# Kernel tuning notes

Hardware: AMD Instinct MI355X
Metric: run time of the kernel (lower is better)

The kernel has to match this reference:

```python
import jax, jax.numpy as jnp
import numpy as np

N, FIN, FOUT, K = 4096, 512, 128, 4
LRELU_ALPHA = 0.2


def setup_inputs() -> dict:
    key = jax.random.key(0)
    k1, k2, k3, k4 = jax.random.split(key, 4)
    x = jax.random.normal(k1, (N, FIN), dtype=jnp.float32)
    # binary adjacency with guaranteed self-loops so every row has a neighbor
    adj = jax.random.randint(k2, (N, N), 0, 2, dtype=jnp.int32)
    adj = jnp.maximum(adj, jnp.eye(N, dtype=jnp.int32))
    # xavier-uniform-ish init for W:(K,FIN,FOUT) and a:(K,2*FOUT,1)
    limW = float(np.sqrt(6.0 / (FIN + FOUT)))
    W = jax.random.uniform(k3, (K, FIN, FOUT), dtype=jnp.float32, minval=-limW, maxval=limW)
    lima = float(np.sqrt(6.0 / (2 * FOUT + 1)))
    a = jax.random.uniform(k4, (K, 2 * FOUT, 1), dtype=jnp.float32, minval=-lima, maxval=lima)
    return {"x": x, "adj": adj, "W": W, "a": a}


def reference(x, adj, W, a):
    # x: [N, Fin], adj: [N, N] int, W: [K, Fin, F'], a: [K, 2F', 1]
    Fout = W.shape[-1]
    h = jnp.einsum('nf,kfo->nko', x, W)          # [N, K, F'] per-head projection
    a_src = a[:, :Fout, 0]                        # [K, F'] acts on h_i
    a_dst = a[:, Fout:, 0]                        # [K, F'] acts on h_j
    # a^T [h_i || h_j] == a_src . h_i + a_dst . h_j  (no O(N^2) concat)
    e_i = jnp.einsum('nko,ko->nk', h, a_src)      # [N, K]
    e_j = jnp.einsum('nko,ko->nk', h, a_dst)      # [N, K]
    scores = e_i[:, :, None] + e_j.T[None, :, :]  # [N, K, N]
    scores = jax.nn.leaky_relu(scores, LRELU_ALPHA)
    mask = (adj != 0)[:, None, :]                 # [N, 1, N]
    scores = jnp.where(mask, scores, -jnp.inf)
    coeffs = jax.nn.softmax(scores, axis=-1)      # [N, K, N]
    # dropout is identity in eval mode
    out = jnp.einsum('nkm,mko->nko', coeffs, h)   # [N, K, F'] aggregation
    return out.reshape(out.shape[0], -1)          # concat heads -> [N, K*F']
```

## Files before the change

kernel.cpp:

```cpp
#include <hip/hip_runtime.h>
#include <hip/hip_bf16.h>

typedef float f4 __attribute__((ext_vector_type(4)));
typedef int   i4 __attribute__((ext_vector_type(4)));
typedef unsigned short us8 __attribute__((ext_vector_type(8)));
typedef short bfrag __attribute__((ext_vector_type(8)));
typedef float f16v __attribute__((ext_vector_type(16)));

constexpr int NN   = 4096;
constexpr int FINc = 512;
constexpr int FOUTc= 128;
constexpr int KHc  = 4;
constexpr int KFc  = 512;
constexpr float ALPHA = 0.2f;
constexpr float LOG2E = 1.44269504088896340736f;

static __device__ __forceinline__ unsigned short f2bf(float f) {
    unsigned u = __float_as_uint(f);
    return (unsigned short)((u + 0x7fffu + ((u >> 16) & 1u)) >> 16);
}
static __device__ __forceinline__ float bf2f(unsigned short u) {
    return __uint_as_float(((unsigned)u) << 16);
}
static __device__ __forceinline__ bfrag us2bf(us8 v) {
    union { us8 u; bfrag s; } cv; cv.u = v; return cv.s;
}


__global__ __launch_bounds__(256) void prep_kernel(const float* __restrict__ x,
                                                   const float* __restrict__ W,
                                                   unsigned short* __restrict__ xb,
                                                   unsigned short* __restrict__ WbT) {
    __shared__ float tile[32 * 132];
    const int b = blockIdx.x, t = threadIdx.x;
    if (b < 1024) {
        size_t base = ((size_t)b * 256 + t) * 8;
        f4 v0 = *(const f4*)&x[base];
        f4 v1 = *(const f4*)&x[base + 4];
        us8 o;
#pragma unroll
        for (int j = 0; j < 4; ++j) { o[j] = f2bf(v0[j]); o[4 + j] = f2bf(v1[j]); }
        *(us8*)&xb[base] = o;
    } else {
        const int wb = b - 1024;
        const int k = wb >> 4, f0 = (wb & 15) * 32;
#pragma unroll
        for (int p = 0; p < 4; ++p) {
            int fl = p * 8 + (t >> 5);
            int oc = (t & 31) * 4;
            *(f4*)&tile[fl * 132 + oc] =
                *(const f4*)&W[(size_t)k * 65536 + (size_t)(f0 + fl) * 128 + oc];
        }
        __syncthreads();
        const int o = t >> 1, fh = (t & 1) * 16;
        alignas(16) unsigned short buf[16];
#pragma unroll
        for (int j = 0; j < 16; ++j) buf[j] = f2bf(tile[(fh + j) * 132 + o]);
        unsigned short* dst = &WbT[((size_t)k * 128 + o) * FINc + f0 + fh];
        *(us8*)dst       = *(const us8*)&buf[0];
        *(us8*)(dst + 8) = *(const us8*)&buf[8];
    }
}

__global__ __launch_bounds__(256) void gemmh_bits_kernel(const unsigned short* __restrict__ xb,
                                                         const unsigned short* __restrict__ WbT,
                                                         const int* __restrict__ adj,
                                                         unsigned short* __restrict__ hB,
                                                         unsigned* __restrict__ bits) {
    __shared__ char Ax[64 * 128];
    __shared__ char Bx[64 * 128];
    const int b = blockIdx.x, t = threadIdx.x;
    if (b >= 512) {
        size_t i0 = (size_t)(b - 512) * 16384 + (size_t)t * 64;
        const int* ap = adj + i0;
        unsigned long long bb = 0ull;
#pragma unroll
        for (int c = 0; c < 16; ++c) {
            i4 v = *(const i4*)(ap + c * 4);
            unsigned n = (v[0] != 0 ? 1u : 0u) | (v[1] != 0 ? 2u : 0u)
                       | (v[2] != 0 ? 4u : 0u) | (v[3] != 0 ? 8u : 0u);
            bb |= (unsigned long long)n << (c * 4);
        }
        *(unsigned long long*)&bits[i0 >> 5] = bb;
        return;
    }
    const int wid = t >> 6, lane = t & 63;
    const int c0 = (b & 7) * 64, n0 = (b >> 3) * 64;
    const int head = c0 >> 7, ob = c0 & 127;
    const int srow = t >> 2, sseg = t & 3;
    const unsigned short* asrc = &xb[(size_t)(n0 + srow) * FINc + sseg * 16];
    const unsigned short* bsrc = &WbT[((size_t)(head * 128 + ob + srow)) * FINc + sseg * 16];
    const int rowbase = (wid & 1) * 32, colbase = (wid >> 1) * 32;
    f16v acc = {};
    for (int fc = 0; fc < FINc; fc += 64) {
        us8 a0 = *(const us8*)(asrc + fc), a1 = *(const us8*)(asrc + fc + 8);
        us8 b0 = *(const us8*)(bsrc + fc), b1 = *(const us8*)(bsrc + fc + 8);
        __syncthreads();
        {
            int byt = (sseg * 32) ^ ((srow & 7) << 4);
            char* pa = Ax + srow * 128;
            *(us8*)(pa + byt) = a0;  *(us8*)(pa + (byt ^ 16)) = a1;
            char* pb = Bx + srow * 128;
            *(us8*)(pb + byt) = b0;  *(us8*)(pb + (byt ^ 16)) = b1;
        }
        __syncthreads();
#pragma unroll
        for (int ks = 0; ks < 4; ++ks) {
            int kb = ks * 32 + ((lane >> 5) << 4);
            int ar = rowbase + (lane & 31);
            bfrag af = *(const bfrag*)(Ax + ar * 128 + (kb ^ ((ar & 7) << 4)));
            int bc = colbase + (lane & 31);
            bfrag bf = *(const bfrag*)(Bx + bc * 128 + (kb ^ ((bc & 7) << 4)));
            acc = __builtin_amdgcn_mfma_f32_32x32x16_bf16(af, bf, acc, 0, 0, 0);
        }
    }
    __syncthreads();
#pragma unroll
    for (int reg = 0; reg < 16; ++reg) {
        int row = rowbase + (reg & 3) + 8 * (reg >> 2) + 4 * (lane >> 5);
        int col = colbase + (lane & 31);
        *(unsigned short*)(Ax + row * 128 + ((col * 2) ^ ((row & 7) << 4))) = f2bf(acc[reg]);
    }
    __syncthreads();
    {
        const int col_l = t & 63;
        unsigned short* dstbase = hB + (size_t)head * 524288 + (size_t)(n0 >> 6) * 8192
                                     + (size_t)(ob + col_l) * 8;
#pragma unroll
        for (int g = 0; g < 2; ++g) {
            int o8 = (t >> 6) + g * 4;
            int ks = o8 >> 1, lg = o8 & 1;
            alignas(16) unsigned short buf[8];
#pragma unroll
            for (int j = 0; j < 8; ++j) {
                int r = o8 * 8 + j;
                buf[j] = *(const unsigned short*)(Ax + r * 128 + ((col_l * 2) ^ ((r & 7) << 4)));
            }
            *(us8*)(dstbase + ks * 2048 + lg * 1024) = *(const us8*)buf;
        }
    }
}

__global__ __launch_bounds__(256) void e2_kernel(const unsigned short* __restrict__ hB,
                                                 const float* __restrict__ a,
                                                 float* __restrict__ ei,
                                                 float* __restrict__ ejT) {
    __shared__ unsigned short hs[8192];
    __shared__ float as[128], ad[128];
    __shared__ float pim[4][64], pjm[4][64];
    const int t = threadIdx.x;
    const int k = blockIdx.x >> 6;
    const int mc = blockIdx.x & 63;
    if (t < 128) as[t] = a[k * 256 + t] * LOG2E;
    else         ad[t - 128] = a[k * 256 + t] * LOG2E;
    const unsigned short* src = hB + ((size_t)k * 64 + mc) * 8192;
#pragma unroll
    for (int i = 0; i < 4; ++i) {
        int off = i * 2048 + t * 8;
        *(us8*)&hs[off] = *(const us8*)&src[off];
    }
    __syncthreads();
    const int m = t & 63, wq = t >> 6;
    const int base = (m >> 4) * 2048 + ((m >> 3) & 1) * 1024 + (m & 7);
    float si = 0.f, sj = 0.f;
#pragma unroll
    for (int cc = 0; cc < 32; ++cc) {
        int c = wq * 32 + cc;
        float v = bf2f(hs[base + c * 8]);
        si += v * as[c];
        sj += v * ad[c];
    }
    pim[wq][m] = si; pjm[wq][m] = sj;
    __syncthreads();
    if (t < 64) {
        ei[(mc * 64 + t) * KHc + k]        = pim[0][t] + pim[1][t] + pim[2][t] + pim[3][t];
        ejT[(size_t)k * NN + mc * 64 + t]  = pjm[0][t] + pjm[1][t] + pjm[2][t] + pjm[3][t];
    }
}

__global__ __launch_bounds__(256, 3) void out_mfma_kernel(const unsigned* __restrict__ bits,
                                                          const float* __restrict__ ei,
                                                          const float* __restrict__ ejT,
                                                          const unsigned short* __restrict__ hB,
                                                          float* __restrict__ pacc,
                                                          float* __restrict__ psum) {
    __shared__ unsigned bitsL[4][544];
    __shared__ float ejL[4][512];
    __shared__ float red[4096];
    __shared__ float sred[4][32];
    const int bid = blockIdx.x;
    const int nb  = (bid & 7) * 128 + (bid >> 3);
    const int k   = nb >> 8;
    const int rt  = (nb & 255) >> 1;
    const int hf  = nb & 1;
    const int n0  = rt * 32;
    const int t = threadIdx.x, lane = t & 63, w = t >> 6;
    const int row = lane & 31, kh = lane >> 5;
    const int mq  = hf * 2048 + w * 512;
    {
        int r = lane >> 1, cb = (lane & 1) * 8;
        const unsigned* src = &bits[(size_t)(n0 + r) * 128 + (mq >> 5) + cb];
        unsigned* dst = &bitsL[w][r * 17 + cb];
#pragma unroll
        for (int c = 0; c < 8; ++c) dst[c] = src[c];
    }
    {
        const float* src = &ejT[(size_t)k * NN + mq + lane * 8];
        *(f4*)&ejL[w][lane * 8]     = *(const f4*)src;
        *(f4*)&ejL[w][lane * 8 + 4] = *(const f4*)(src + 4);
    }
    const float eiv = ei[(n0 + row) * KHc + k];
    const char* hbase = (const char*)hB + (size_t)k * 1048576 + (size_t)(mq >> 6) * 16384
                        + kh * 2048 + row * 16;
    bfrag ones;
#pragma unroll
    for (int j = 0; j < 8; ++j) ones[j] = (short)0x3F80;
    f16v acc0 = {}, acc1 = {}, acc2 = {}, acc3 = {}, accs = {};

    for (int it = 0; it < 8; ++it) {
        const char* hc = hbase + (size_t)it * 16384;
        unsigned bw0 = bitsL[w][row * 17 + it * 2];
        unsigned bw1 = bitsL[w][row * 17 + it * 2 + 1];
#pragma unroll
        for (int ks = 0; ks < 4; ++ks) {
            us8 hg0 = *(const us8*)(hc + ks * 4096);
            us8 hg1 = *(const us8*)(hc + ks * 4096 + 512);
            us8 hg2 = *(const us8*)(hc + ks * 4096 + 1024);
            us8 hg3 = *(const us8*)(hc + ks * 4096 + 1536);
            f4 ej0 = *(const f4*)&ejL[w][it * 64 + ks * 16 + kh * 8];
            f4 ej1 = *(const f4*)&ejL[w][it * 64 + ks * 16 + kh * 8 + 4];
            unsigned bw = ((ks & 2) ? bw1 : bw0) >> ((ks & 1) * 16 + kh * 8);
            float p[8];
#pragma unroll
            for (int j = 0; j < 8; ++j) {
                float sc = eiv + (j < 4 ? ej0[j] : ej1[j - 4]);
                sc = fmaxf(sc, ALPHA * sc);
                float pp = exp2f(sc);
                p[j] = ((bw >> j) & 1) ? pp : 0.f;
            }
            union { unsigned u[4]; bfrag s; } pk;
#pragma unroll
            for (int j = 0; j < 4; ++j) {
                float2 fp; fp.x = p[2 * j]; fp.y = p[2 * j + 1];
                __hip_bfloat162 b2 = __float22bfloat162_rn(fp);
                pk.u[j] = *reinterpret_cast<unsigned*>(&b2);
            }
            acc0 = __builtin_amdgcn_mfma_f32_32x32x16_bf16(pk.s, us2bf(hg0), acc0, 0, 0, 0);
            acc1 = __builtin_amdgcn_mfma_f32_32x32x16_bf16(pk.s, us2bf(hg1), acc1, 0, 0, 0);
            acc2 = __builtin_amdgcn_mfma_f32_32x32x16_bf16(pk.s, us2bf(hg2), acc2, 0, 0, 0);
            acc3 = __builtin_amdgcn_mfma_f32_32x32x16_bf16(pk.s, us2bf(hg3), acc3, 0, 0, 0);
            accs = __builtin_amdgcn_mfma_f32_32x32x16_bf16(pk.s, ones, accs, 0, 0, 0);
        }
    }
    if (row == 0) {
#pragma unroll
        for (int reg = 0; reg < 16; ++reg) {
            int r = (reg & 3) + 8 * (reg >> 2) + 4 * kh;
            sred[w][r] = accs[reg];
        }
    }
    __syncthreads();
    if (t < 32) psum[(size_t)nb * 32 + t] =
        (sred[0][t] + sred[1][t]) + (sred[2][t] + sred[3][t]);
#pragma unroll
    for (int src = 1; src < 4; ++src) {
        if (w == src) {
#pragma unroll
            for (int cg = 0; cg < 4; ++cg) {
                const f16v& av = (cg == 0) ? acc0 : (cg == 1) ? acc1 : (cg == 2) ? acc2 : acc3;
#pragma unroll
                for (int reg = 0; reg < 16; ++reg) {
                    int r = (reg & 3) + 8 * (reg >> 2) + 4 * kh;
                    red[r * 128 + cg * 32 + row] = av[reg];
                }
            }
        }
        __syncthreads();
        if (w == 0) {
#pragma unroll
            for (int cg = 0; cg < 4; ++cg) {
                f16v& av = (cg == 0) ? acc0 : (cg == 1) ? acc1 : (cg == 2) ? acc2 : acc3;
#pragma unroll
                for (int reg = 0; reg < 16; ++reg) {
                    int r = (reg & 3) + 8 * (reg >> 2) + 4 * kh;
                    av[reg] += red[r * 128 + cg * 32 + row];
                }
            }
        }
        __syncthreads();
    }
    if (w == 0) {
        float* pa = &pacc[(size_t)nb * 4096];
#pragma unroll
        for (int cg = 0; cg < 4; ++cg) {
            const f16v& av = (cg == 0) ? acc0 : (cg == 1) ? acc1 : (cg == 2) ? acc2 : acc3;
#pragma unroll
            for (int reg = 0; reg < 16; ++reg) {
                int r = (reg & 3) + 8 * (reg >> 2) + 4 * kh;
                pa[r * 128 + cg * 32 + row] = av[reg];
            }
        }
    }
}

__global__ __launch_bounds__(256) void combine_kernel(const float* __restrict__ pacc,
                                                      const float* __restrict__ psum,
                                                      float* __restrict__ out) {
    const int b = blockIdx.x;
    const int k = b >> 7, rt = b & 127;
    const int t = threadIdx.x;
    const int row = t >> 3, cb = (t & 7) * 16;
    const float* a0 = &pacc[(size_t)(b * 2) * 4096 + row * 128 + cb];
    const float* a1 = a0 + 4096;
    float s = psum[(size_t)(b * 2) * 32 + row] + psum[(size_t)(b * 2 + 1) * 32 + row];
    float rinv = 1.0f / s;
    float* o = &out[(size_t)(rt * 32 + row) * KFc + k * FOUTc + cb];
#pragma unroll
    for (int c4 = 0; c4 < 4; ++c4) {
        f4 v0 = *(const f4*)(a0 + c4 * 4);
        f4 v1 = *(const f4*)(a1 + c4 * 4);
        f4 v;
#pragma unroll
        for (int j = 0; j < 4; ++j) v[j] = (v0[j] + v1[j]) * rinv;
        *(f4*)(o + c4 * 4) = v;
    }
}

extern "C" void kernel_launch(void* const* d_in, const int* in_sizes, int n_in,
                              void* d_out, int out_size, void* d_ws, size_t ws_size,
                              hipStream_t stream) {
    const float* x   = (const float*)d_in[0];
    const int*   adj = (const int*)d_in[1];
    const float* W   = (const float*)d_in[2];
    const float* a   = (const float*)d_in[3];
    float* out = (float*)d_out;
    char* ws = (char*)d_ws;

    unsigned short* hB   = (unsigned short*)ws;
    unsigned short* xb   = (unsigned short*)(ws + (4u << 20));
    float*          pacc = (float*)(ws + (4u << 20));
    unsigned short* WbT  = (unsigned short*)(ws + (20u << 20));
    unsigned*       bits = (unsigned*)(ws + (21u << 20));
    float*          ei   = (float*)(ws + (23u << 20));
    float*          ejT  = ei + (size_t)NN * KHc;
    float*          psum = ejT + (size_t)NN * KHc;

    prep_kernel<<<1088, 256, 0, stream>>>(x, W, xb, WbT);
    gemmh_bits_kernel<<<1536, 256, 0, stream>>>(xb, WbT, adj, hB, bits);
    e2_kernel<<<256, 256, 0, stream>>>(hB, a, ei, ejT);
    out_mfma_kernel<<<1024, 256, 0, stream>>>(bits, ei, ejT, hB, pacc, psum);
    combine_kernel<<<512, 256, 0, stream>>>(pacc, psum, out);
}
```

Measured before the change: 79.39 us.

## Factor exp out of inner loop and fuse combine via atomic ticket

Precomputes exp2 of the destination scores for both leaky-ReLU branches. Because exp2 is monotonic, each weight becomes max(ejP, C*ejN) with a per-row constant, which removes the per-element exp2 and select from the MFMA loop. The mask is applied with a bitwise AND against a small LDS table. The separate combine kernel is removed: the last-finishing block of each pair normalizes and writes the output, coordinated by an atomic ticket that the prep kernel zeroes. Without max-subtraction the exponentials carry a risk of overflow or precision loss, and the ticket adds a fence and atomic per block.

```diff
diff --git a/kernel.cpp b/kernel.cpp
--- a/kernel.cpp
+++ b/kernel.cpp
@@ -12,7 +12,6 @@
 constexpr int FOUTc= 128;
 constexpr int KHc  = 4;
 constexpr int KFc  = 512;
-constexpr float ALPHA = 0.2f;
 constexpr float LOG2E = 1.44269504088896340736f;
 
 static __device__ __forceinline__ unsigned short f2bf(float f) {
@@ -30,7 +29,8 @@
 __global__ __launch_bounds__(256) void prep_kernel(const float* __restrict__ x,
                                                    const float* __restrict__ W,
                                                    unsigned short* __restrict__ xb,
-                                                   unsigned short* __restrict__ WbT) {
+                                                   unsigned short* __restrict__ WbT,
+                                                   unsigned* __restrict__ ticket) {
     __shared__ float tile[32 * 132];
     const int b = blockIdx.x, t = threadIdx.x;
     if (b < 1024) {
@@ -41,7 +41,7 @@
 #pragma unroll
         for (int j = 0; j < 4; ++j) { o[j] = f2bf(v0[j]); o[4 + j] = f2bf(v1[j]); }
         *(us8*)&xb[base] = o;
-    } else {
+    } else if (b < 1088) {
         const int wb = b - 1024;
         const int k = wb >> 4, f0 = (wb & 15) * 32;
 #pragma unroll
@@ -59,6 +59,9 @@
         unsigned short* dst = &WbT[((size_t)k * 128 + o) * FINc + f0 + fh];
         *(us8*)dst       = *(const us8*)&buf[0];
         *(us8*)(dst + 8) = *(const us8*)&buf[8];
+    } else {
+        ticket[t] = 0u;
+        ticket[t + 256] = 0u;
     }
 }
 
@@ -144,7 +147,8 @@
 __global__ __launch_bounds__(256) void e2_kernel(const unsigned short* __restrict__ hB,
                                                  const float* __restrict__ a,
                                                  float* __restrict__ ei,
-                                                 float* __restrict__ ejT) {
+                                                 float* __restrict__ ejP,
+                                                 float* __restrict__ ejN) {
     __shared__ unsigned short hs[8192];
     __shared__ float as[128], ad[128];
     __shared__ float pim[4][64], pjm[4][64];
@@ -173,21 +177,32 @@
     pim[wq][m] = si; pjm[wq][m] = sj;
     __syncthreads();
     if (t < 64) {
-        ei[(mc * 64 + t) * KHc + k]        = pim[0][t] + pim[1][t] + pim[2][t] + pim[3][t];
-        ejT[(size_t)k * NN + mc * 64 + t]  = pjm[0][t] + pjm[1][t] + pjm[2][t] + pjm[3][t];
+        float siv = pim[0][t] + pim[1][t] + pim[2][t] + pim[3][t];
+        float sjv = pjm[0][t] + pjm[1][t] + pjm[2][t] + pjm[3][t];
+        ei[(mc * 64 + t) * KHc + k]       = siv;
+        ejP[(size_t)k * NN + mc * 64 + t] = exp2f(sjv);
+        ejN[(size_t)k * NN + mc * 64 + t] = exp2f(0.2f * sjv);
     }
 }
 
 __global__ __launch_bounds__(256, 3) void out_mfma_kernel(const unsigned* __restrict__ bits,
                                                           const float* __restrict__ ei,
-                                                          const float* __restrict__ ejT,
+                                                          const float* __restrict__ ejP,
+                                                          const float* __restrict__ ejN,
                                                           const unsigned short* __restrict__ hB,
                                                           float* __restrict__ pacc,
-                                                          float* __restrict__ psum) {
+                                                          float* __restrict__ psum,
+                                                          unsigned* __restrict__ ticket,
+                                                          float* __restrict__ out) {
+    __shared__ float arena[4096];
     __shared__ unsigned bitsL[4][544];
-    __shared__ float ejL[4][512];
-    __shared__ float red[4096];
+    __shared__ unsigned mtab[4][4];
     __shared__ float sred[4][32];
+    __shared__ unsigned oldt_s;
+    float* ejPL = arena;
+    float* ejNL = arena + 2048;
+    float* red  = arena;
+
     const int bid = blockIdx.x;
     const int nb  = (bid & 7) * 128 + (bid >> 3);
     const int k   = nb >> 8;
@@ -197,6 +212,7 @@
     const int t = threadIdx.x, lane = t & 63, w = t >> 6;
     const int row = lane & 31, kh = lane >> 5;
     const int mq  = hf * 2048 + w * 512;
+    if (lane < 4) mtab[w][lane] = ((lane & 1) ? 0xFFFFu : 0u) | ((lane & 2) ? 0xFFFF0000u : 0u);
     {
         int r = lane >> 1, cb = (lane & 1) * 8;
         const unsigned* src = &bits[(size_t)(n0 + r) * 128 + (mq >> 5) + cb];
@@ -205,11 +221,15 @@
         for (int c = 0; c < 8; ++c) dst[c] = src[c];
     }
     {
-        const float* src = &ejT[(size_t)k * NN + mq + lane * 8];
-        *(f4*)&ejL[w][lane * 8]     = *(const f4*)src;
-        *(f4*)&ejL[w][lane * 8 + 4] = *(const f4*)(src + 4);
+        const float* sp = &ejP[(size_t)k * NN + mq + lane * 8];
+        const float* sn = &ejN[(size_t)k * NN + mq + lane * 8];
+        *(f4*)&ejPL[w * 512 + lane * 8]     = *(const f4*)sp;
+        *(f4*)&ejPL[w * 512 + lane * 8 + 4] = *(const f4*)(sp + 4);
+        *(f4*)&ejNL[w * 512 + lane * 8]     = *(const f4*)sn;
+        *(f4*)&ejNL[w * 512 + lane * 8 + 4] = *(const f4*)(sn + 4);
     }
     const float eiv = ei[(n0 + row) * KHc + k];
+    const float C = exp2f(-0.8f * eiv);
     const char* hbase = (const char*)hB + (size_t)k * 1048576 + (size_t)(mq >> 6) * 16384
                         + kh * 2048 + row * 16;
     bfrag ones;
@@ -219,31 +239,32 @@
 
     for (int it = 0; it < 8; ++it) {
         const char* hc = hbase + (size_t)it * 16384;
-        unsigned bw0 = bitsL[w][row * 17 + it * 2];
-        unsigned bw1 = bitsL[w][row * 17 + it * 2 + 1];
+        unsigned bwA = bitsL[w][row * 17 + it * 2];
+        unsigned bwB = bitsL[w][row * 17 + it * 2 + 1];
 #pragma unroll
         for (int ks = 0; ks < 4; ++ks) {
             us8 hg0 = *(const us8*)(hc + ks * 4096);
             us8 hg1 = *(const us8*)(hc + ks * 4096 + 512);
             us8 hg2 = *(const us8*)(hc + ks * 4096 + 1024);
             us8 hg3 = *(const us8*)(hc + ks * 4096 + 1536);
-            f4 ej0 = *(const f4*)&ejL[w][it * 64 + ks * 16 + kh * 8];
-            f4 ej1 = *(const f4*)&ejL[w][it * 64 + ks * 16 + kh * 8 + 4];
-            unsigned bw = ((ks & 2) ? bw1 : bw0) >> ((ks & 1) * 16 + kh * 8);
-            float p[8];
-#pragma unroll
-            for (int j = 0; j < 8; ++j) {
-                float sc = eiv + (j < 4 ? ej0[j] : ej1[j - 4]);
-                sc = fmaxf(sc, ALPHA * sc);
-                float pp = exp2f(sc);
-                p[j] = ((bw >> j) & 1) ? pp : 0.f;
-            }
+            const int eb = w * 512 + it * 64 + ks * 16 + kh * 8;
+            f4 jp0 = *(const f4*)&ejPL[eb];
+            f4 jp1 = *(const f4*)&ejPL[eb + 4];
+            f4 jn0 = *(const f4*)&ejNL[eb];
+            f4 jn1 = *(const f4*)&ejNL[eb + 4];
+            unsigned bw = ((ks & 2) ? bwB : bwA) >> ((ks & 1) * 16 + kh * 8);
             union { unsigned u[4]; bfrag s; } pk;
 #pragma unroll
-            for (int j = 0; j < 4; ++j) {
-                float2 fp; fp.x = p[2 * j]; fp.y = p[2 * j + 1];
+            for (int jj = 0; jj < 4; ++jj) {
+                float a0 = (jj < 2) ? jp0[2 * jj]     : jp1[2 * jj - 4];
+                float a1 = (jj < 2) ? jp0[2 * jj + 1] : jp1[2 * jj - 3];
+                float b0 = (jj < 2) ? jn0[2 * jj]     : jn1[2 * jj - 4];
+                float b1 = (jj < 2) ? jn0[2 * jj + 1] : jn1[2 * jj - 3];
+                float m0 = fmaxf(a0, C * b0);
+                float m1 = fmaxf(a1, C * b1);
+                float2 fp; fp.x = m0; fp.y = m1;
                 __hip_bfloat162 b2 = __float22bfloat162_rn(fp);
-                pk.u[j] = *reinterpret_cast<unsigned*>(&b2);
+                pk.u[jj] = (*reinterpret_cast<unsigned*>(&b2)) & mtab[w][(bw >> (2 * jj)) & 3];
             }
             acc0 = __builtin_amdgcn_mfma_f32_32x32x16_bf16(pk.s, us2bf(hg0), acc0, 0, 0, 0);
             acc1 = __builtin_amdgcn_mfma_f32_32x32x16_bf16(pk.s, us2bf(hg1), acc1, 0, 0, 0);
@@ -301,28 +322,28 @@
             }
         }
     }
-}
-
-__global__ __launch_bounds__(256) void combine_kernel(const float* __restrict__ pacc,
-                                                      const float* __restrict__ psum,
-                                                      float* __restrict__ out) {
-    const int b = blockIdx.x;
-    const int k = b >> 7, rt = b & 127;
-    const int t = threadIdx.x;
-    const int row = t >> 3, cb = (t & 7) * 16;
-    const float* a0 = &pacc[(size_t)(b * 2) * 4096 + row * 128 + cb];
-    const float* a1 = a0 + 4096;
-    float s = psum[(size_t)(b * 2) * 32 + row] + psum[(size_t)(b * 2 + 1) * 32 + row];
-    float rinv = 1.0f / s;
-    float* o = &out[(size_t)(rt * 32 + row) * KFc + k * FOUTc + cb];
-#pragma unroll
-    for (int c4 = 0; c4 < 4; ++c4) {
-        f4 v0 = *(const f4*)(a0 + c4 * 4);
-        f4 v1 = *(const f4*)(a1 + c4 * 4);
-        f4 v;
-#pragma unroll
-        for (int j = 0; j < 4; ++j) v[j] = (v0[j] + v1[j]) * rinv;
-        *(f4*)(o + c4 * 4) = v;
+    __threadfence();
+    __syncthreads();
+    if (t == 0) oldt_s = atomicAdd(&ticket[nb >> 1], 1u);
+    __syncthreads();
+    if (oldt_s == 1u) {
+        __threadfence();
+        const int p0 = nb & ~1, p1 = nb | 1;
+        const int rr = t >> 3, cb = (t & 7) * 16;
+        float s = psum[(size_t)p0 * 32 + rr] + psum[(size_t)p1 * 32 + rr];
+        float rinv = 1.0f / s;
+        const float* a0p = &pacc[(size_t)p0 * 4096 + rr * 128 + cb];
+        const float* a1p = &pacc[(size_t)p1 * 4096 + rr * 128 + cb];
+        float* o = &out[(size_t)(n0 + rr) * KFc + k * FOUTc + cb];
+#pragma unroll
+        for (int c4 = 0; c4 < 4; ++c4) {
+            f4 v0 = *(const f4*)(a0p + c4 * 4);
+            f4 v1 = *(const f4*)(a1p + c4 * 4);
+            f4 v;
+#pragma unroll
+            for (int j = 0; j < 4; ++j) v[j] = (v0[j] + v1[j]) * rinv;
+            *(f4*)(o + c4 * 4) = v;
+        }
     }
 }
 
@@ -342,12 +363,13 @@
     unsigned short* WbT  = (unsigned short*)(ws + (20u << 20));
     unsigned*       bits = (unsigned*)(ws + (21u << 20));
     float*          ei   = (float*)(ws + (23u << 20));
-    float*          ejT  = ei + (size_t)NN * KHc;
-    float*          psum = ejT + (size_t)NN * KHc;
-
-    prep_kernel<<<1088, 256, 0, stream>>>(x, W, xb, WbT);
+    float*          ejP  = ei + (size_t)NN * KHc;
+    float*          ejN  = ejP + (size_t)NN * KHc;
+    float*          psum = ejN + (size_t)NN * KHc;
+    unsigned*       ticket = (unsigned*)(psum + (size_t)1024 * 32);
+
+    prep_kernel<<<1089, 256, 0, stream>>>(x, W, xb, WbT, ticket);
     gemmh_bits_kernel<<<1536, 256, 0, stream>>>(xb, WbT, adj, hB, bits);
-    e2_kernel<<<256, 256, 0, stream>>>(hB, a, ei, ejT);
-    out_mfma_kernel<<<1024, 256, 0, stream>>>(bits, ei, ejT, hB, pacc, psum);
-    combine_kernel<<<512, 256, 0, stream>>>(pacc, psum, out);
-}
+    e2_kernel<<<256, 256, 0, stream>>>(hB, a, ei, ejP, ejN);
+    out_mfma_kernel<<<1024, 256, 0, stream>>>(bits, ei, ejP, ejN, hB, pacc, psum, ticket, out);
+}
```

After: 238.6 us. +200.6%, slower.

## Fuse combine into attention kernel by covering full neighbor range per block

Applied to the files above, without the earlier changes.

Each out_mfma block now covers all 4096 neighbors for its 32-row tile and head, instead of splitting them into two halves. Because of that, normalisation and the final store happen in the same kernel, and the separate combine kernel plus the pacc/psum round-trip through memory are removed. The ej staging buffer is reused as the reduction buffer to save LDS. The cost is half as many blocks (512) with twice the serial loop length, and launch bounds drop to 2 blocks per SM, which reduces parallelism and occupancy.

```diff
diff --git a/kernel.cpp b/kernel.cpp
--- a/kernel.cpp
+++ b/kernel.cpp
@@ -178,36 +178,34 @@
     }
 }
 
-__global__ __launch_bounds__(256, 3) void out_mfma_kernel(const unsigned* __restrict__ bits,
+__global__ __launch_bounds__(256, 2) void out_mfma_kernel(const unsigned* __restrict__ bits,
                                                           const float* __restrict__ ei,
                                                           const float* __restrict__ ejT,
                                                           const unsigned short* __restrict__ hB,
-                                                          float* __restrict__ pacc,
-                                                          float* __restrict__ psum) {
-    __shared__ unsigned bitsL[4][544];
-    __shared__ float ejL[4][512];
-    __shared__ float red[4096];
+                                                          float* __restrict__ out) {
+    __shared__ unsigned bitsL[4][1056];
+    __shared__ float ejred[4096];
     __shared__ float sred[4][32];
+    __shared__ float lsum[32];
     const int bid = blockIdx.x;
-    const int nb  = (bid & 7) * 128 + (bid >> 3);
-    const int k   = nb >> 8;
-    const int rt  = (nb & 255) >> 1;
-    const int hf  = nb & 1;
-    const int n0  = rt * 32;
+    const int nb  = (bid & 7) * 64 + (bid >> 3);
+    const int k   = nb >> 7;
+    const int n0  = (nb & 127) * 32;
     const int t = threadIdx.x, lane = t & 63, w = t >> 6;
     const int row = lane & 31, kh = lane >> 5;
-    const int mq  = hf * 2048 + w * 512;
+    const int mq  = w * 1024;
     {
-        int r = lane >> 1, cb = (lane & 1) * 8;
+        int r = lane >> 1, cb = (lane & 1) * 16;
         const unsigned* src = &bits[(size_t)(n0 + r) * 128 + (mq >> 5) + cb];
-        unsigned* dst = &bitsL[w][r * 17 + cb];
-#pragma unroll
-        for (int c = 0; c < 8; ++c) dst[c] = src[c];
+        unsigned* dst = &bitsL[w][r * 33 + cb];
+#pragma unroll
+        for (int c = 0; c < 16; ++c) dst[c] = src[c];
     }
     {
-        const float* src = &ejT[(size_t)k * NN + mq + lane * 8];
-        *(f4*)&ejL[w][lane * 8]     = *(const f4*)src;
-        *(f4*)&ejL[w][lane * 8 + 4] = *(const f4*)(src + 4);
+        const float* src = &ejT[(size_t)k * NN + mq + lane * 16];
+        float* dst = &ejred[w * 1024 + lane * 16];
+#pragma unroll
+        for (int c = 0; c < 4; ++c) *(f4*)(dst + c * 4) = *(const f4*)(src + c * 4);
     }
     const float eiv = ei[(n0 + row) * KHc + k];
     const char* hbase = (const char*)hB + (size_t)k * 1048576 + (size_t)(mq >> 6) * 16384
@@ -217,19 +215,20 @@
     for (int j = 0; j < 8; ++j) ones[j] = (short)0x3F80;
     f16v acc0 = {}, acc1 = {}, acc2 = {}, acc3 = {}, accs = {};
 
-    for (int it = 0; it < 8; ++it) {
+    for (int it = 0; it < 16; ++it) {
         const char* hc = hbase + (size_t)it * 16384;
-        unsigned bw0 = bitsL[w][row * 17 + it * 2];
-        unsigned bw1 = bitsL[w][row * 17 + it * 2 + 1];
+        unsigned bwA = bitsL[w][row * 33 + it * 2];
+        unsigned bwB = bitsL[w][row * 33 + it * 2 + 1];
 #pragma unroll
         for (int ks = 0; ks < 4; ++ks) {
             us8 hg0 = *(const us8*)(hc + ks * 4096);
             us8 hg1 = *(const us8*)(hc + ks * 4096 + 512);
             us8 hg2 = *(const us8*)(hc + ks * 4096 + 1024);
             us8 hg3 = *(const us8*)(hc + ks * 4096 + 1536);
-            f4 ej0 = *(const f4*)&ejL[w][it * 64 + ks * 16 + kh * 8];
-            f4 ej1 = *(const f4*)&ejL[w][it * 64 + ks * 16 + kh * 8 + 4];
-            unsigned bw = ((ks & 2) ? bw1 : bw0) >> ((ks & 1) * 16 + kh * 8);
+            const int eb = w * 1024 + it * 64 + ks * 16 + kh * 8;
+            f4 ej0 = *(const f4*)&ejred[eb];
+            f4 ej1 = *(const f4*)&ejred[eb + 4];
+            unsigned bw = ((ks & 2) ? bwB : bwA) >> ((ks & 1) * 16 + kh * 8);
             float p[8];
 #pragma unroll
             for (int j = 0; j < 8; ++j) {
@@ -260,8 +259,8 @@
         }
     }
     __syncthreads();
-    if (t < 32) psum[(size_t)nb * 32 + t] =
-        (sred[0][t] + sred[1][t]) + (sred[2][t] + sred[3][t]);
+    if (t < 32) lsum[t] = 1.0f / ((sred[0][t] + sred[1][t]) + (sred[2][t] + sred[3][t]));
+    float* red = ejred;
 #pragma unroll
     for (int src = 1; src < 4; ++src) {
         if (w == src) {
@@ -290,39 +289,15 @@
         __syncthreads();
     }
     if (w == 0) {
-        float* pa = &pacc[(size_t)nb * 4096];
 #pragma unroll
         for (int cg = 0; cg < 4; ++cg) {
             const f16v& av = (cg == 0) ? acc0 : (cg == 1) ? acc1 : (cg == 2) ? acc2 : acc3;
 #pragma unroll
             for (int reg = 0; reg < 16; ++reg) {
                 int r = (reg & 3) + 8 * (reg >> 2) + 4 * kh;
-                pa[r * 128 + cg * 32 + row] = av[reg];
-            }
-        }
-    }
-}
-
-__global__ __launch_bounds__(256) void combine_kernel(const float* __restrict__ pacc,
-                                                      const float* __restrict__ psum,
-                                                      float* __restrict__ out) {
-    const int b = blockIdx.x;
-    const int k = b >> 7, rt = b & 127;
-    const int t = threadIdx.x;
-    const int row = t >> 3, cb = (t & 7) * 16;
-    const float* a0 = &pacc[(size_t)(b * 2) * 4096 + row * 128 + cb];
-    const float* a1 = a0 + 4096;
-    float s = psum[(size_t)(b * 2) * 32 + row] + psum[(size_t)(b * 2 + 1) * 32 + row];
-    float rinv = 1.0f / s;
-    float* o = &out[(size_t)(rt * 32 + row) * KFc + k * FOUTc + cb];
-#pragma unroll
-    for (int c4 = 0; c4 < 4; ++c4) {
-        f4 v0 = *(const f4*)(a0 + c4 * 4);
-        f4 v1 = *(const f4*)(a1 + c4 * 4);
-        f4 v;
-#pragma unroll
-        for (int j = 0; j < 4; ++j) v[j] = (v0[j] + v1[j]) * rinv;
-        *(f4*)(o + c4 * 4) = v;
+                out[(size_t)(n0 + r) * KFc + k * FOUTc + cg * 32 + row] = av[reg] * lsum[r];
+            }
+        }
     }
 }
 
@@ -338,16 +313,13 @@
 
     unsigned short* hB   = (unsigned short*)ws;
     unsigned short* xb   = (unsigned short*)(ws + (4u << 20));
-    float*          pacc = (float*)(ws + (4u << 20));
     unsigned short* WbT  = (unsigned short*)(ws + (20u << 20));
     unsigned*       bits = (unsigned*)(ws + (21u << 20));
     float*          ei   = (float*)(ws + (23u << 20));
     float*          ejT  = ei + (size_t)NN * KHc;
-    float*          psum = ejT + (size_t)NN * KHc;
 
     prep_kernel<<<1088, 256, 0, stream>>>(x, W, xb, WbT);
     gemmh_bits_kernel<<<1536, 256, 0, stream>>>(xb, WbT, adj, hB, bits);
     e2_kernel<<<256, 256, 0, stream>>>(hB, a, ei, ejT);
-    out_mfma_kernel<<<1024, 256, 0, stream>>>(bits, ei, ejT, hB, pacc, psum);
-    combine_kernel<<<512, 256, 0, stream>>>(pacc, psum, out);
-}
+    out_mfma_kernel<<<512, 256, 0, stream>>>(bits, ei, ejT, hB, out);
+}
```

After: 78.53 us. No clear change (-1.1%).
